# Performance work log

Measured on AMD Instinct MI355X. Metric: run time of the kernel, lower is better.

Reference implementation:

```python
import jax, jax.numpy as jnp
import numpy as np

D_MODEL = 1024
N_HEADS = 16
D_K = D_MODEL // N_HEADS


def setup_inputs() -> dict:
    key = jax.random.key(0)
    ks = jax.random.split(key, 12)
    B, S, D, H = 2, 2048, D_MODEL, N_HEADS
    s = 1.0 / np.sqrt(D)
    inp = {
        "x": jax.random.normal(ks[0], (B, S, D), jnp.float32),
        "Wq": jax.random.normal(ks[1], (D, D), jnp.float32) * s,
        "bq": jnp.zeros((D,), jnp.float32),
        "Wk": jax.random.normal(ks[2], (D, D), jnp.float32) * s,
        "bk": jnp.zeros((D,), jnp.float32),
        "Wv": jax.random.normal(ks[3], (D, D), jnp.float32) * s,
        "bv": jnp.zeros((D,), jnp.float32),
        "Wo": jax.random.normal(ks[4], (D, D), jnp.float32) * s,
        "bo": jnp.zeros((D,), jnp.float32),
        "Wp": jax.random.normal(ks[5], (D, H), jnp.float32) * s,
        "bp": jnp.zeros((H,), jnp.float32),
        "alpha": jax.random.normal(ks[6], (H,), jnp.float32) * 0.1,
    }
    return inp


def reference(x, Wq, bq, Wk, bk, Wv, bv, Wo, bo, Wp, bp, alpha):
    B, S, D = x.shape
    H, dk = N_HEADS, D_K
    scale = dk ** -0.5
    # projections -> (B, H, S, dk)
    Q = (x @ Wq + bq).reshape(B, S, H, dk).transpose(0, 2, 1, 3)
    K = (x @ Wk + bk).reshape(B, S, H, dk).transpose(0, 2, 1, 3)
    V = (x @ Wv + bv).reshape(B, S, H, dk).transpose(0, 2, 1, 3)
    scores = jnp.einsum("bhid,bhjd->bhij", Q, K) * scale  # (B,H,S,S)
    # phase derived from x: (B,S,H) -> (B,H,S)
    phase = (x @ Wp + bp).transpose(0, 2, 1)
    # coherence(i,j) = cos(phi_i - phi_j), per batch/head
    coherence = jnp.cos(phase[:, :, :, None] - phase[:, :, None, :])
    scores = scores + alpha[None, :, None, None] * coherence
    attn = jax.nn.softmax(scores, axis=-1)
    out = jnp.einsum("bhij,bhjd->bhid", attn, V)  # (B,H,S,dk)
    out = out.transpose(0, 2, 1, 3).reshape(B, S, D)
    return out @ Wo + bo
```

## Files before the change

kernel.cpp:

```cpp
#include <hip/hip_runtime.h>
#include <math.h>


#define S_LEN 2048
#define NHEADS 16

typedef __attribute__((ext_vector_type(8))) short short8;
typedef __attribute__((ext_vector_type(4))) float floatx4;
typedef __attribute__((ext_vector_type(16))) float floatx16;

__device__ inline unsigned short f2bf(float f) {
    union { float f; unsigned int i; } v; v.f = f;
    unsigned int u = v.i;
    return (unsigned short)((u + 0x7fffu + ((u >> 16) & 1u)) >> 16);
}
__device__ inline unsigned int pack2_bf16(float hi, float lo) {
    union { float f; unsigned int u; } a, b; a.f = hi; b.f = lo;
    return __builtin_amdgcn_perm(a.u, b.u, 0x07060302u);
}
__device__ inline void async_copy16(const unsigned short* src, unsigned short* dst_lds) {
    __builtin_amdgcn_global_load_lds(
        (const __attribute__((address_space(1))) unsigned int*)(src),
        (__attribute__((address_space(3))) unsigned int*)(dst_lds), 16, 0, 0);
}
__device__ inline floatx16 zero16() {
    floatx16 v;
#pragma unroll
    for (int i = 0; i < 16; i++) v[i] = 0.f;
    return v;
}

__global__ __launch_bounds__(256) void prep_kernel(
    const float* __restrict__ x, const float* __restrict__ Wp,
    const float* __restrict__ bp, const float* __restrict__ alpha,
    const float* __restrict__ w0, const float* __restrict__ w1,
    const float* __restrict__ w2, const float* __restrict__ w3,
    unsigned short* __restrict__ d0, unsigned short* __restrict__ d1,
    unsigned short* __restrict__ d2, unsigned short* __restrict__ d3,
    unsigned short* __restrict__ qcs, unsigned short* __restrict__ kcs,
    unsigned short* __restrict__ xb) {
    __shared__ __align__(16) unsigned short shmem[64 * 72];
    int t = threadIdx.x;
    if (blockIdx.x < 4096) {
        float* red = reinterpret_cast<float*>(shmem);
        int bid = blockIdx.x;
        int b = bid >> 11, s = bid & 2047;
        int h = t & 15, c = t >> 4;
        const float* xr = x + (size_t)bid * 1024;
        {
            float4 xv = *reinterpret_cast<const float4*>(&xr[t * 4]);
            uint2 o;
            o.x = (unsigned int)f2bf(xv.x) | ((unsigned int)f2bf(xv.y) << 16);
            o.y = (unsigned int)f2bf(xv.z) | ((unsigned int)f2bf(xv.w) << 16);
            *reinterpret_cast<uint2*>(&xb[(size_t)bid * 1024 + t * 4]) = o;
        }
        float acc = 0.f;
#pragma unroll 8
        for (int kk = 0; kk < 64; kk++) {
            int k = c * 64 + kk;
            acc += xr[k] * Wp[k * 16 + h];
        }
        red[t] = acc;
        __syncthreads();
        if (t < 16) {
            float sum = 0.f;
#pragma unroll
            for (int c2 = 0; c2 < 16; c2++) sum += red[c2 * 16 + t];
            sum += bp[t];
            float sv, cv;
            __sincosf(sum, &sv, &cv);
            float as = alpha[t] * 1.44269504f;
            size_t off = ((size_t)(b * NHEADS + t) * S_LEN + s) * 16;
            uint4 qv = make_uint4(
                (unsigned int)f2bf(as * cv) | ((unsigned int)f2bf(as * sv) << 16), 0u, 0u, 0u);
            uint4 kv = make_uint4(
                (unsigned int)f2bf(cv) | ((unsigned int)f2bf(sv) << 16), 0u, 0u, 0u);
            uint4 z = make_uint4(0u, 0u, 0u, 0u);
            *reinterpret_cast<uint4*>(&qcs[off]) = qv;
            *reinterpret_cast<uint4*>(&qcs[off + 8]) = z;
            *reinterpret_cast<uint4*>(&kcs[off]) = kv;
            *reinterpret_cast<uint4*>(&kcs[off + 8]) = z;
        }
    } else {
        unsigned short (*tile)[72] = reinterpret_cast<unsigned short (*)[72]>(shmem);
        int bid = blockIdx.x - 4096;
        int mat = bid >> 8;
        int tl  = bid & 255;
        int tr = tl >> 4, tc = tl & 15;
        const float* src    = (mat == 0) ? w0 : (mat == 1) ? w1 : (mat == 2) ? w2 : w3;
        unsigned short* dst = (mat == 0) ? d0 : (mat == 1) ? d1 : (mat == 2) ? d2 : d3;
        int col = t & 63, rbase = (t >> 6) * 16;
#pragma unroll
        for (int i = 0; i < 16; i++) {
            int row = rbase + i;
            tile[row][col] = f2bf(src[(size_t)(tr * 64 + row) * 1024 + tc * 64 + col]);
        }
        __syncthreads();
#pragma unroll
        for (int i = 0; i < 16; i++) {
            int row = rbase + i;
            dst[(size_t)(tc * 64 + row) * 1024 + tr * 64 + col] = tile[col][row];
        }
    }
}

template <int MT>
__global__ __launch_bounds__(256) void gemm_bt(
    const unsigned short* __restrict__ A, const unsigned short* __restrict__ BT,
    int N, int mode,
    const float* __restrict__ b0, const float* __restrict__ b1,
    const float* __restrict__ b2,
    unsigned short* __restrict__ o0, unsigned short* __restrict__ o1,
    unsigned short* __restrict__ o2, float* __restrict__ of) {
    __shared__ __align__(16) unsigned short As[MT * 32];
    __shared__ __align__(16) unsigned short Bs[128 * 32];
    const int K = 1024;
    const int MI = MT / 32;
    int t = threadIdx.x;
    int mBase = blockIdx.x * MT;
    int nBase = blockIdx.y * 128;
    int w = t >> 6, lane = t & 63, l15 = lane & 15, quad = lane >> 4;
    int wm = (w & 1) * (MT / 2), wn = (w >> 1) * 64;
    floatx4 acc[MI][4];
#pragma unroll
    for (int i = 0; i < MI; i++)
#pragma unroll
        for (int j = 0; j < 4; j++) acc[i][j] = (floatx4){0.f, 0.f, 0.f, 0.f};

    int arow = t >> 2, aseg = (t & 3) * 8;
    for (int k0 = 0; k0 < K; k0 += 32) {
        __syncthreads();
#pragma unroll
        for (int i = 0; i < MT / 64; i++)
            async_copy16(&A[(size_t)(mBase + i * 64 + arow) * K + k0 + aseg],
                         &As[(i * 64 + arow) * 32 + aseg]);
#pragma unroll
        for (int i = 0; i < 2; i++)
            async_copy16(&BT[(size_t)(nBase + i * 64 + arow) * K + k0 + aseg],
                         &Bs[(i * 64 + arow) * 32 + aseg]);
        __syncthreads();
        short8 af[MI], bfr[4];
#pragma unroll
        for (int mi = 0; mi < MI; mi++)
            af[mi] = *reinterpret_cast<const short8*>(&As[(wm + mi * 16 + l15) * 32 + quad * 8]);
#pragma unroll
        for (int ni = 0; ni < 4; ni++)
            bfr[ni] = *reinterpret_cast<const short8*>(&Bs[(wn + ni * 16 + l15) * 32 + quad * 8]);
#pragma unroll
        for (int mi = 0; mi < MI; mi++)
#pragma unroll
            for (int ni = 0; ni < 4; ni++)
                acc[mi][ni] = __builtin_amdgcn_mfma_f32_16x16x32_bf16(af[mi], bfr[ni], acc[mi][ni], 0, 0, 0);
    }

#pragma unroll
    for (int mi = 0; mi < MI; mi++) {
        int rowB = mBase + wm + mi * 16 + quad * 4;
#pragma unroll
        for (int ni = 0; ni < 4; ni++) {
            int col = nBase + wn + ni * 16 + l15;
            if (mode == 0) {
                float bias = b0[col];
#pragma unroll
                for (int r = 0; r < 4; r++) {
                    of[(size_t)(rowB + r) * N + col] = acc[mi][ni][r] + bias;
                }
            } else {
                int mat = col >> 10, nn = col & 1023;
                int h = nn >> 6, d = nn & 63;
                int b = rowB >> 11, sidx = rowB & 2047;
                if (mat == 2) {
                    float bv = b2[nn];
                    unsigned int lo = (unsigned int)f2bf(acc[mi][ni][0] + bv) |
                                      ((unsigned int)f2bf(acc[mi][ni][1] + bv) << 16);
                    unsigned int hi = (unsigned int)f2bf(acc[mi][ni][2] + bv) |
                                      ((unsigned int)f2bf(acc[mi][ni][3] + bv) << 16);
                    int jj = sidx & 15;
                    int s23 = ((jj & 4) << 1) | ((jj & 8) >> 1);
                    size_t rowOff = ((size_t)((b * NHEADS + h) * 64 + d)) * S_LEN +
                                    (sidx & ~15) + s23;
                    *reinterpret_cast<uint2*>(&o2[rowOff]) = make_uint2(lo, hi);
                } else {
                    const float* bias  = (mat == 0) ? b0 : b1;
                    unsigned short* op = (mat == 0) ? o0 : o1;
                    float bv = bias[nn];
                    float scl = (mat == 0) ? 0.18033688f : 1.0f;
#pragma unroll
                    for (int r = 0; r < 4; r++) {
                        float cv = (acc[mi][ni][r] + bv) * scl;
                        op[(((size_t)b * NHEADS + h) * S_LEN + (sidx + r)) * 64 + d] = f2bf(cv);
                    }
                }
            }
        }
    }
}

__global__ __launch_bounds__(256) void attn_kernel(
    const unsigned short* __restrict__ Qg, const unsigned short* __restrict__ Qcs,
    const unsigned short* __restrict__ Kg, const unsigned short* __restrict__ Kcs,
    const unsigned short* __restrict__ VTg, unsigned short* __restrict__ ctx) {
    __shared__ __align__(16) unsigned short KdB[2][4096];
    __shared__ __align__(16) unsigned short KcB[2][1024];
    __shared__ __align__(16) unsigned short VtB[2][4096];

    int bid = blockIdx.x;
    int bh = bid >> 4, qt = bid & 15;
    int t = threadIdx.x, lane = t & 63, w = t >> 6;
    int l31 = lane & 31, g = lane >> 5;
    int i0w = qt * 128 + w * 32;
    size_t base = (size_t)bh * (S_LEN * 64);
    size_t basec = (size_t)bh * (S_LEN * 16);

    short8 qd[4], qc;
    {
        const unsigned short* qrow = Qg + base + (size_t)(i0w + l31) * 64;
#pragma unroll
        for (int f = 0; f < 4; f++)
            qd[f] = *reinterpret_cast<const short8*>(qrow + f * 16 + g * 8);
        qc = *reinterpret_cast<const short8*>(Qcs + basec + (size_t)(i0w + l31) * 16 + g * 8);
    }

    int srow = t >> 3;
    int scol = (((t & 7) - ((srow >> 2) & 7)) & 7) * 8;
    const unsigned short* kd0 = Kg + base + (size_t)srow * 64 + scol;
    const unsigned short* kd1 = Kg + base + (size_t)(srow + 32) * 64 + scol;
    const unsigned short* vv0 = VTg + base + (size_t)srow * S_LEN + scol;
    const unsigned short* vv1 = VTg + base + (size_t)(srow + 32) * S_LEN + scol;
    const unsigned short* kcc = Kcs + basec + t * 8;

    async_copy16(kd0, &KdB[0][t * 8]);
    async_copy16(kd1, &KdB[0][2048 + t * 8]);
    async_copy16(vv0, &VtB[0][t * 8]);
    async_copy16(vv1, &VtB[0][2048 + t * 8]);
    if (t < 128) async_copy16(kcc, &KcB[0][t * 8]);

    floatx16 o0 = zero16(), o1 = zero16(), lac = zero16();
    const short8 ones8 = {(short)0x3F80, (short)0x3F80, (short)0x3F80, (short)0x3F80,
                          (short)0x3F80, (short)0x3F80, (short)0x3F80, (short)0x3F80};

    int rot = (l31 >> 2) & 7;
    int fo[4];
#pragma unroll
    for (int f = 0; f < 4; f++) fo[f] = ((2 * f + g + rot) & 7) * 8;
    int arow = l31 * 64;
    int kcof = l31 * 16 + g * 8;

    for (int kt = 0; kt < 32; kt++) {
        int p = kt & 1;
        __syncthreads();
        if (kt < 31) {
            int kn = kt + 1, pn = p ^ 1;
            async_copy16(kd0 + kn * 4096, &KdB[pn][t * 8]);
            async_copy16(kd1 + kn * 4096, &KdB[pn][2048 + t * 8]);
            async_copy16(vv0 + kn * 64, &VtB[pn][t * 8]);
            async_copy16(vv1 + kn * 64, &VtB[pn][2048 + t * 8]);
            if (t < 128) async_copy16(kcc + kn * 1024, &KcB[pn][t * 8]);
        }

        short8 pf[4];
#pragma unroll
        for (int jt = 0; jt < 2; jt++) {
            const unsigned short* kb = &KdB[p][jt * 2048 + arow];
            floatx16 st = zero16();
            st = __builtin_amdgcn_mfma_f32_32x32x16_bf16(
                *reinterpret_cast<const short8*>(kb + fo[0]), qd[0], st, 0, 0, 0);
            st = __builtin_amdgcn_mfma_f32_32x32x16_bf16(
                *reinterpret_cast<const short8*>(kb + fo[1]), qd[1], st, 0, 0, 0);
            st = __builtin_amdgcn_mfma_f32_32x32x16_bf16(
                *reinterpret_cast<const short8*>(kb + fo[2]), qd[2], st, 0, 0, 0);
            st = __builtin_amdgcn_mfma_f32_32x32x16_bf16(
                *reinterpret_cast<const short8*>(kb + fo[3]), qd[3], st, 0, 0, 0);
            st = __builtin_amdgcn_mfma_f32_32x32x16_bf16(
                *reinterpret_cast<const short8*>(&KcB[p][jt * 512 + kcof]), qc, st, 0, 0, 0);
            float pe[16];
#pragma unroll
            for (int r = 0; r < 16; r++) pe[r] = __builtin_amdgcn_exp2f(st[r]);
#pragma unroll
            for (int h = 0; h < 2; h++) {
                union { unsigned int u[4]; short8 s; } pk;
                pk.u[0] = pack2_bf16(pe[8 * h + 1], pe[8 * h + 0]);
                pk.u[1] = pack2_bf16(pe[8 * h + 3], pe[8 * h + 2]);
                pk.u[2] = pack2_bf16(pe[8 * h + 5], pe[8 * h + 4]);
                pk.u[3] = pack2_bf16(pe[8 * h + 7], pe[8 * h + 6]);
                pf[2 * jt + h] = pk.s;
            }
        }

#pragma unroll
        for (int c = 0; c < 4; c++) {
            lac = __builtin_amdgcn_mfma_f32_32x32x16_bf16(pf[c], ones8, lac, 0, 0, 0);
            int vo = ((2 * c + g + rot) & 7) * 8;
            short8 vf0 = *reinterpret_cast<const short8*>(&VtB[p][arow + vo]);
            short8 vf1 = *reinterpret_cast<const short8*>(&VtB[p][2048 + arow + vo]);
            o0 = __builtin_amdgcn_mfma_f32_32x32x16_bf16(pf[c], vf0, o0, 0, 0, 0);
            o1 = __builtin_amdgcn_mfma_f32_32x32x16_bf16(pf[c], vf1, o1, 0, 0, 0);
        }
    }

    int b = bh >> 4, h = bh & 15;
#pragma unroll
    for (int r = 0; r < 16; r++) {
        int i = i0w + (r & 3) + 8 * (r >> 2) + 4 * g;
        float inv = 1.0f / lac[r];
        size_t off = ((size_t)(b * S_LEN + i)) * 1024 + h * 64;
        ctx[off + l31]      = f2bf(o0[r] * inv);
        ctx[off + 32 + l31] = f2bf(o1[r] * inv);
    }
}

extern "C" void kernel_launch(void* const* d_in, const int* in_sizes, int n_in,
                              void* d_out, int out_size, void* d_ws, size_t ws_size,
                              hipStream_t stream) {
    const float* x     = (const float*)d_in[0];
    const float* Wq    = (const float*)d_in[1];
    const float* bq    = (const float*)d_in[2];
    const float* Wk    = (const float*)d_in[3];
    const float* bk    = (const float*)d_in[4];
    const float* Wv    = (const float*)d_in[5];
    const float* bv    = (const float*)d_in[6];
    const float* Wo    = (const float*)d_in[7];
    const float* bo    = (const float*)d_in[8];
    const float* Wp    = (const float*)d_in[9];
    const float* bp    = (const float*)d_in[10];
    const float* alpha = (const float*)d_in[11];
    float* out = (float*)d_out;

    const size_t MB = 1048576;
    char* ws = (char*)d_ws;
    unsigned short* WT   = (unsigned short*)(ws);
    unsigned short* WoT  = (unsigned short*)(ws + 6 * MB);
    unsigned short* xb   = (unsigned short*)(ws + 8 * MB);
    unsigned short* ctx  = (unsigned short*)(ws + 8 * MB);
    unsigned short* Qw   = (unsigned short*)(ws + 16 * MB);
    unsigned short* Kw   = (unsigned short*)(ws + 24 * MB);
    unsigned short* VTg  = (unsigned short*)(ws + 32 * MB);
    unsigned short* Qcs  = (unsigned short*)(ws + 40 * MB);
    unsigned short* Kcs  = (unsigned short*)(ws + 42 * MB);

    prep_kernel<<<dim3(5120), dim3(256), 0, stream>>>(
        x, Wp, bp, alpha, Wq, Wk, Wv, Wo,
        WT, WT + 1048576, WT + 2097152, WoT, Qcs, Kcs, xb);
    gemm_bt<128><<<dim3(32, 24), dim3(256), 0, stream>>>(
        xb, WT, 3072, 1, bq, bk, bv, Qw, Kw, VTg, (float*)nullptr);
    attn_kernel<<<dim3(512), dim3(256), 0, stream>>>(
        Qw, Qcs, Kw, Kcs, VTg, ctx);
    gemm_bt<64><<<dim3(64, 8), dim3(256), 0, stream>>>(
        ctx, WoT, 1024, 0, bo, bo, bo,
        (unsigned short*)nullptr, (unsigned short*)nullptr,
        (unsigned short*)nullptr, out);
}
```

Before: 230.9 us.

## Split attention KV loop across two wave groups and widen GEMM k-step

The attention kernel now launches 512 threads per block. Two halves each process half of the key/value tiles with their own double buffers, and the partial outputs and row sums are combined through shared memory at the end. This doubles the waves per query tile, which should help hide latency on a grid of only 512 blocks, at the cost of a final reduction and more LDS. The projection GEMMs now load 64-wide k slices with a rotated (swizzled) LDS layout. That halves the number of barrier pairs per K loop and is meant to reduce bank conflicts, but it uses more shared memory per block.

```diff
diff --git a/kernel.cpp b/kernel.cpp
--- a/kernel.cpp
+++ b/kernel.cpp
@@ -112,8 +112,8 @@
     const float* __restrict__ b2,
     unsigned short* __restrict__ o0, unsigned short* __restrict__ o1,
     unsigned short* __restrict__ o2, float* __restrict__ of) {
-    __shared__ __align__(16) unsigned short As[MT * 32];
-    __shared__ __align__(16) unsigned short Bs[128 * 32];
+    __shared__ __align__(16) unsigned short As[MT * 64];
+    __shared__ __align__(16) unsigned short Bs[128 * 64];
     const int K = 1024;
     const int MI = MT / 32;
     int t = threadIdx.x;
@@ -127,30 +127,37 @@
 #pragma unroll
         for (int j = 0; j < 4; j++) acc[i][j] = (floatx4){0.f, 0.f, 0.f, 0.f};
 
-    int arow = t >> 2, aseg = (t & 3) * 8;
-    for (int k0 = 0; k0 < K; k0 += 32) {
-        __syncthreads();
-#pragma unroll
-        for (int i = 0; i < MT / 64; i++)
-            async_copy16(&A[(size_t)(mBase + i * 64 + arow) * K + k0 + aseg],
-                         &As[(i * 64 + arow) * 32 + aseg]);
-#pragma unroll
-        for (int i = 0; i < 2; i++)
-            async_copy16(&BT[(size_t)(nBase + i * 64 + arow) * K + k0 + aseg],
-                         &Bs[(i * 64 + arow) * 32 + aseg]);
-        __syncthreads();
-        short8 af[MI], bfr[4];
-#pragma unroll
-        for (int mi = 0; mi < MI; mi++)
-            af[mi] = *reinterpret_cast<const short8*>(&As[(wm + mi * 16 + l15) * 32 + quad * 8]);
-#pragma unroll
-        for (int ni = 0; ni < 4; ni++)
-            bfr[ni] = *reinterpret_cast<const short8*>(&Bs[(wn + ni * 16 + l15) * 32 + quad * 8]);
-#pragma unroll
-        for (int mi = 0; mi < MI; mi++)
+    int srow = t >> 3, sseg = t & 7;
+    int scol = ((sseg - (srow & 7)) & 7) * 8;
+    int rotf = l15 & 7;
+
+    for (int k0 = 0; k0 < K; k0 += 64) {
+        __syncthreads();
+#pragma unroll
+        for (int i = 0; i < MT / 32; i++)
+            async_copy16(&A[(size_t)(mBase + i * 32 + srow) * K + k0 + scol],
+                         &As[i * 2048 + t * 8]);
+#pragma unroll
+        for (int i = 0; i < 4; i++)
+            async_copy16(&BT[(size_t)(nBase + i * 32 + srow) * K + k0 + scol],
+                         &Bs[i * 2048 + t * 8]);
+        __syncthreads();
+#pragma unroll
+        for (int kk = 0; kk < 2; kk++) {
+            int gr = ((kk * 4 + quad + rotf) & 7) * 8;
+            short8 af[MI], bfr[4];
+#pragma unroll
+            for (int mi = 0; mi < MI; mi++)
+                af[mi] = *reinterpret_cast<const short8*>(&As[(wm + mi * 16 + l15) * 64 + gr]);
 #pragma unroll
             for (int ni = 0; ni < 4; ni++)
-                acc[mi][ni] = __builtin_amdgcn_mfma_f32_16x16x32_bf16(af[mi], bfr[ni], acc[mi][ni], 0, 0, 0);
+                bfr[ni] = *reinterpret_cast<const short8*>(&Bs[(wn + ni * 16 + l15) * 64 + gr]);
+#pragma unroll
+            for (int mi = 0; mi < MI; mi++)
+#pragma unroll
+                for (int ni = 0; ni < 4; ni++)
+                    acc[mi][ni] = __builtin_amdgcn_mfma_f32_16x16x32_bf16(af[mi], bfr[ni], acc[mi][ni], 0, 0, 0);
+        }
     }
 
 #pragma unroll
@@ -196,19 +203,19 @@
     }
 }
 
-__global__ __launch_bounds__(256) void attn_kernel(
+__global__ __launch_bounds__(512, 4) void attn_kernel(
     const unsigned short* __restrict__ Qg, const unsigned short* __restrict__ Qcs,
     const unsigned short* __restrict__ Kg, const unsigned short* __restrict__ Kcs,
     const unsigned short* __restrict__ VTg, unsigned short* __restrict__ ctx) {
-    __shared__ __align__(16) unsigned short KdB[2][4096];
-    __shared__ __align__(16) unsigned short KcB[2][1024];
-    __shared__ __align__(16) unsigned short VtB[2][4096];
+    __shared__ __align__(16) unsigned short smem[36864];
 
     int bid = blockIdx.x;
     int bh = bid >> 4, qt = bid & 15;
-    int t = threadIdx.x, lane = t & 63, w = t >> 6;
+    int t = threadIdx.x, lane = t & 63;
+    int half = t >> 8, th = t & 255;
+    int cg = (t >> 6) & 3;
     int l31 = lane & 31, g = lane >> 5;
-    int i0w = qt * 128 + w * 32;
+    int i0w = qt * 128 + cg * 32;
     size_t base = (size_t)bh * (S_LEN * 64);
     size_t basec = (size_t)bh * (S_LEN * 16);
 
@@ -221,58 +228,69 @@
         qc = *reinterpret_cast<const short8*>(Qcs + basec + (size_t)(i0w + l31) * 16 + g * 8);
     }
 
-    int srow = t >> 3;
-    int scol = (((t & 7) - ((srow >> 2) & 7)) & 7) * 8;
+    int srow = th >> 3, sseg = th & 7;
+    int scol = ((sseg - (srow & 7)) & 7) * 8;
     const unsigned short* kd0 = Kg + base + (size_t)srow * 64 + scol;
     const unsigned short* kd1 = Kg + base + (size_t)(srow + 32) * 64 + scol;
     const unsigned short* vv0 = VTg + base + (size_t)srow * S_LEN + scol;
     const unsigned short* vv1 = VTg + base + (size_t)(srow + 32) * S_LEN + scol;
-    const unsigned short* kcc = Kcs + basec + t * 8;
-
-    async_copy16(kd0, &KdB[0][t * 8]);
-    async_copy16(kd1, &KdB[0][2048 + t * 8]);
-    async_copy16(vv0, &VtB[0][t * 8]);
-    async_copy16(vv1, &VtB[0][2048 + t * 8]);
-    if (t < 128) async_copy16(kcc, &KcB[0][t * 8]);
+    const unsigned short* kcc = Kcs + basec + th * 8;
+
+    unsigned short* KD0 = smem + (half * 2) * 4096;
+    unsigned short* KD1 = smem + (half * 2 + 1) * 4096;
+    unsigned short* VT0 = smem + 16384 + (half * 2) * 4096;
+    unsigned short* VT1 = smem + 16384 + (half * 2 + 1) * 4096;
+    unsigned short* KC0 = smem + 32768 + (half * 2) * 1024;
+    unsigned short* KC1 = smem + 32768 + (half * 2 + 1) * 1024;
+
+    int kt0 = half * 16;
+    {
+        async_copy16(kd0 + (size_t)kt0 * 4096, KD0 + th * 8);
+        async_copy16(kd1 + (size_t)kt0 * 4096, KD0 + 2048 + th * 8);
+        async_copy16(vv0 + kt0 * 64, VT0 + th * 8);
+        async_copy16(vv1 + kt0 * 64, VT0 + 2048 + th * 8);
+        if (th < 128) async_copy16(kcc + (size_t)kt0 * 1024, KC0 + th * 8);
+    }
 
     floatx16 o0 = zero16(), o1 = zero16(), lac = zero16();
     const short8 ones8 = {(short)0x3F80, (short)0x3F80, (short)0x3F80, (short)0x3F80,
                           (short)0x3F80, (short)0x3F80, (short)0x3F80, (short)0x3F80};
 
-    int rot = (l31 >> 2) & 7;
-    int fo[4];
-#pragma unroll
-    for (int f = 0; f < 4; f++) fo[f] = ((2 * f + g + rot) & 7) * 8;
+    int rot = l31 & 7;
+    int kcof = l31 * 16 + g * 8;
     int arow = l31 * 64;
-    int kcof = l31 * 16 + g * 8;
-
-    for (int kt = 0; kt < 32; kt++) {
-        int p = kt & 1;
-        __syncthreads();
-        if (kt < 31) {
-            int kn = kt + 1, pn = p ^ 1;
-            async_copy16(kd0 + kn * 4096, &KdB[pn][t * 8]);
-            async_copy16(kd1 + kn * 4096, &KdB[pn][2048 + t * 8]);
-            async_copy16(vv0 + kn * 64, &VtB[pn][t * 8]);
-            async_copy16(vv1 + kn * 64, &VtB[pn][2048 + t * 8]);
-            if (t < 128) async_copy16(kcc + kn * 1024, &KcB[pn][t * 8]);
+
+    for (int it = 0; it < 16; it++) {
+        int p = it & 1;
+        unsigned short* KDp = p ? KD1 : KD0;
+        unsigned short* VTp = p ? VT1 : VT0;
+        unsigned short* KCp = p ? KC1 : KC0;
+        __syncthreads();
+        if (it < 15) {
+            int kn = kt0 + it + 1;
+            unsigned short* KDn = p ? KD0 : KD1;
+            unsigned short* VTn = p ? VT0 : VT1;
+            unsigned short* KCn = p ? KC0 : KC1;
+            async_copy16(kd0 + (size_t)kn * 4096, KDn + th * 8);
+            async_copy16(kd1 + (size_t)kn * 4096, KDn + 2048 + th * 8);
+            async_copy16(vv0 + kn * 64, VTn + th * 8);
+            async_copy16(vv1 + kn * 64, VTn + 2048 + th * 8);
+            if (th < 128) async_copy16(kcc + (size_t)kn * 1024, KCn + th * 8);
         }
 
         short8 pf[4];
 #pragma unroll
         for (int jt = 0; jt < 2; jt++) {
-            const unsigned short* kb = &KdB[p][jt * 2048 + arow];
+            const unsigned short* kb = KDp + jt * 2048 + arow;
             floatx16 st = zero16();
+#pragma unroll
+            for (int f = 0; f < 4; f++) {
+                int fo = ((2 * f + g + rot) & 7) * 8;
+                st = __builtin_amdgcn_mfma_f32_32x32x16_bf16(
+                    *reinterpret_cast<const short8*>(kb + fo), qd[f], st, 0, 0, 0);
+            }
             st = __builtin_amdgcn_mfma_f32_32x32x16_bf16(
-                *reinterpret_cast<const short8*>(kb + fo[0]), qd[0], st, 0, 0, 0);
-            st = __builtin_amdgcn_mfma_f32_32x32x16_bf16(
-                *reinterpret_cast<const short8*>(kb + fo[1]), qd[1], st, 0, 0, 0);
-            st = __builtin_amdgcn_mfma_f32_32x32x16_bf16(
-                *reinterpret_cast<const short8*>(kb + fo[2]), qd[2], st, 0, 0, 0);
-            st = __builtin_amdgcn_mfma_f32_32x32x16_bf16(
-                *reinterpret_cast<const short8*>(kb + fo[3]), qd[3], st, 0, 0, 0);
-            st = __builtin_amdgcn_mfma_f32_32x32x16_bf16(
-                *reinterpret_cast<const short8*>(&KcB[p][jt * 512 + kcof]), qc, st, 0, 0, 0);
+                *reinterpret_cast<const short8*>(KCp + jt * 512 + kcof), qc, st, 0, 0, 0);
             float pe[16];
 #pragma unroll
             for (int r = 0; r < 16; r++) pe[r] = __builtin_amdgcn_exp2f(st[r]);
@@ -291,21 +309,42 @@
         for (int c = 0; c < 4; c++) {
             lac = __builtin_amdgcn_mfma_f32_32x32x16_bf16(pf[c], ones8, lac, 0, 0, 0);
             int vo = ((2 * c + g + rot) & 7) * 8;
-            short8 vf0 = *reinterpret_cast<const short8*>(&VtB[p][arow + vo]);
-            short8 vf1 = *reinterpret_cast<const short8*>(&VtB[p][2048 + arow + vo]);
+            short8 vf0 = *reinterpret_cast<const short8*>(VTp + arow + vo);
+            short8 vf1 = *reinterpret_cast<const short8*>(VTp + 2048 + arow + vo);
             o0 = __builtin_amdgcn_mfma_f32_32x32x16_bf16(pf[c], vf0, o0, 0, 0, 0);
             o1 = __builtin_amdgcn_mfma_f32_32x32x16_bf16(pf[c], vf1, o1, 0, 0, 0);
         }
     }
 
-    int b = bh >> 4, h = bh & 15;
-#pragma unroll
-    for (int r = 0; r < 16; r++) {
-        int i = i0w + (r & 3) + 8 * (r >> 2) + 4 * g;
-        float inv = 1.0f / lac[r];
-        size_t off = ((size_t)(b * S_LEN + i)) * 1024 + h * 64;
-        ctx[off + l31]      = f2bf(o0[r] * inv);
-        ctx[off + 32 + l31] = f2bf(o1[r] * inv);
+    float* xch = reinterpret_cast<float*>(smem);
+    __syncthreads();
+    if (half == 1) {
+        int xb2 = cg * 3072 + lane;
+#pragma unroll
+        for (int r = 0; r < 16; r++) {
+            xch[xb2 + r * 64]        = o0[r];
+            xch[xb2 + (16 + r) * 64] = o1[r];
+            xch[xb2 + (32 + r) * 64] = lac[r];
+        }
+    }
+    __syncthreads();
+    if (half == 0) {
+        int xb2 = cg * 3072 + lane;
+#pragma unroll
+        for (int r = 0; r < 16; r++) {
+            o0[r] += xch[xb2 + r * 64];
+            o1[r] += xch[xb2 + (16 + r) * 64];
+            lac[r] += xch[xb2 + (32 + r) * 64];
+        }
+        int b = bh >> 4, h = bh & 15;
+#pragma unroll
+        for (int r = 0; r < 16; r++) {
+            int i = i0w + (r & 3) + 8 * (r >> 2) + 4 * g;
+            float inv = 1.0f / lac[r];
+            size_t off = ((size_t)(b * S_LEN + i)) * 1024 + h * 64;
+            ctx[off + l31]      = f2bf(o0[r] * inv);
+            ctx[off + 32 + l31] = f2bf(o1[r] * inv);
+        }
     }
 }
 
@@ -343,7 +382,7 @@
         WT, WT + 1048576, WT + 2097152, WoT, Qcs, Kcs, xb);
     gemm_bt<128><<<dim3(32, 24), dim3(256), 0, stream>>>(
         xb, WT, 3072, 1, bq, bk, bv, Qw, Kw, VTg, (float*)nullptr);
-    attn_kernel<<<dim3(512), dim3(256), 0, stream>>>(
+    attn_kernel<<<dim3(512), dim3(512), 0, stream>>>(
         Qw, Qcs, Kw, Kcs, VTg, ctx);
     gemm_bt<64><<<dim3(64, 8), dim3(256), 0, stream>>>(
         ctx, WoT, 1024, 0, bo, bo, bo,
```

Result: faster. 224.3 us (-2.9%).
